# Optimization experiments

Measured on AMD Instinct MI355X. Metric: run time of the kernel, lower is better.

## Reference

```python
import jax, jax.numpy as jnp
import numpy as np

N = 4096      # num_nodes
U = 64        # num_units
IN = 2        # input_dim
DIM = U + IN  # 66
H = 4         # attention heads
ALPHA = 0.2   # leaky slope inside attention scores
SLOPE = 0.01  # nn.LeakyReLU() default for subnet activations
NEG_INF = -9e15


def setup_inputs() -> dict:
    key = jax.random.key(0)
    ks = jax.random.split(key, 20)
    def gn(k, shape, fan):
        return jax.random.normal(k, shape, dtype=jnp.float32) / np.float32(np.sqrt(fan))
    adj = jax.random.randint(ks[2], (N, N), 0, 2, dtype=jnp.int32)
    adj = jnp.maximum(adj, jnp.eye(N, dtype=jnp.int32))  # ensure self-loops
    return {
        "inputs": jax.random.normal(ks[0], (1, N * IN), dtype=jnp.float32),
        "hx": jax.random.normal(ks[1], (1, N, U), dtype=jnp.float32),
        "adj": adj,
        "m1_W": gn(ks[3], (H, DIM, DIM), DIM),
        "m1_a1": gn(ks[4], (H, DIM), DIM),
        "m1_a2": gn(ks[5], (H, DIM), DIM),
        "m1_Wout": gn(ks[6], (H * DIM, DIM), H * DIM),
        "m1_ao1": gn(ks[7], (DIM,), DIM),
        "m1_ao2": gn(ks[8], (DIM,), DIM),
        "m2_W": gn(ks[9], (H, DIM, DIM), DIM),
        "m2_a1": gn(ks[10], (H, DIM), DIM),
        "m2_a2": gn(ks[11], (H, DIM), DIM),
        "m2_Wout": gn(ks[12], (H * DIM, DIM), H * DIM),
        "m2_ao1": gn(ks[13], (DIM,), DIM),
        "m2_ao2": gn(ks[14], (DIM,), DIM),
        "g1_W": gn(ks[15], (DIM, 2 * U), DIM),
        "g1_b": jnp.zeros((2 * U,), dtype=jnp.float32),
        "g2_W": gn(ks[16], (DIM, U), DIM),
        "g2_b": jnp.zeros((U,), dtype=jnp.float32),
    }


def gat_layer(x, W, a1, a2, mask):
    # x: [N,Fin], W: [Fin,Fout], a1/a2: [Fout], mask: [N,N] bool
    h = x @ W                                   # [N,Fout]
    f1 = h @ a1                                 # [N] source term
    f2 = h @ a2                                 # [N] target term
    e = jax.nn.leaky_relu(f1[:, None] + f2[None, :], ALPHA)  # [N,N]
    e = jnp.where(mask, e, NEG_INF)
    attn = jax.nn.softmax(e, axis=-1)
    return attn @ h                             # [N,Fout]


def subnet(x, W, a1, a2, Wout, ao1, ao2, mask):
    # multi-head GAT, concat heads, activation, output GAT layer, activation
    heads = jax.vmap(gat_layer, in_axes=(None, 0, 0, 0, None))(x, W, a1, a2, mask)  # [H,N,DIM]
    hcat = jnp.transpose(heads, (1, 0, 2)).reshape(x.shape[0], -1)                   # [N,H*DIM]
    hcat = jax.nn.leaky_relu(hcat, SLOPE)
    out = gat_layer(hcat, Wout, ao1, ao2, mask)                                      # [N,DIM]
    return jax.nn.leaky_relu(out, SLOPE)


def reference(inputs, hx, adj, m1_W, m1_a1, m1_a2, m1_Wout, m1_ao1, m1_ao2,
              m2_W, m2_a1, m2_a2, m2_Wout, m2_ao1, m2_ao2,
              g1_W, g1_b, g2_W, g2_b):
    mask = adj > 0
    xi = inputs.reshape(N, IN)
    xh = hx.reshape(N, U)
    # _GAT1: concat(inputs, hx) -> GATSubNet1 -> linear -> sigmoid -> split r,u
    x1 = jnp.concatenate([xi, xh], axis=-1)                 # [N,DIM]
    g1 = subnet(x1, m1_W, m1_a1, m1_a2, m1_Wout, m1_ao1, m1_ao2, mask)
    value = jax.nn.sigmoid(g1 @ g1_W + g1_b)                # [N,2U]
    r, u = value[:, :U], value[:, U:]
    # _GAT2: concat(inputs, r*hx) -> GATSubNet2 -> linear -> tanh
    x2 = jnp.concatenate([xi, r * xh], axis=-1)             # [N,DIM]
    g2 = subnet(x2, m2_W, m2_a1, m2_a2, m2_Wout, m2_ao1, m2_ao2, mask)
    c = jnp.tanh(g2 @ g2_W + g2_b)                          # [N,U]
    new_state = u * xh + (1.0 - u) * c
    return new_state.reshape(1, N, U)
```

## Files before the change

kernel.cpp:

```cpp
#include <hip/hip_runtime.h>
#include <hip/hip_bf16.h>

constexpr int kN = 4096;
constexpr int kDim = 66;
constexpr int kH = 4;
constexpr int kU = 64;
constexpr float kAlpha = 0.2f;
constexpr float kSlope = 0.01f;
constexpr float kLog2e = 1.44269504f;

typedef _Float16 half8 __attribute__((ext_vector_type(8)));
typedef _Float16 half2t __attribute__((ext_vector_type(2)));
typedef __attribute__((ext_vector_type(4))) float floatx4;

__device__ inline unsigned int fkey(float f){
  unsigned int u = __float_as_uint(f);
  return (u & 0x80000000u) ? ~u : (u | 0x80000000u);
}
__device__ inline float funkey(unsigned int k){
  unsigned int u = (k & 0x80000000u) ? (k ^ 0x80000000u) : ~k;
  return __uint_as_float(u);
}

__global__ void setup_k(const int* __restrict__ adj, unsigned long long* __restrict__ packed,
                        const float* __restrict__ in2, const float* __restrict__ hx,
                        _Float16* __restrict__ x1b, _Float16* __restrict__ x2b,
                        const float* __restrict__ m1W, const float* __restrict__ m1a1, const float* __restrict__ m1a2,
                        const float* __restrict__ m1Wo, const float* __restrict__ m1ao1, const float* __restrict__ m1ao2,
                        const float* __restrict__ m2W, const float* __restrict__ m2a1, const float* __restrict__ m2a2,
                        const float* __restrict__ m2Wo, const float* __restrict__ m2ao1, const float* __restrict__ m2ao2,
                        const float* __restrict__ g1W, const float* __restrict__ g1b,
                        const float* __restrict__ g2W, const float* __restrict__ g2b,
                        _Float16* __restrict__ B1t, _Float16* __restrict__ B1t2,
                        _Float16* __restrict__ B2t, _Float16* __restrict__ B2t2,
                        _Float16* __restrict__ Bgt, _Float16* __restrict__ Bft,
                        unsigned int* __restrict__ fmaxbuf){
  int bb = blockIdx.x, t = threadIdx.x;
  if (bb < 16384){
    int gid = bb * 256 + t;
    unsigned long long m = __ballot(adj[gid] != 0);
    if ((t & 63) == 0) packed[gid >> 6] = m;
    return;
  }
  if (bb < 16384 + 1024){
    int i = (bb - 16384) * 4 + (t >> 6);
    int c = t & 63;
    x1b[(size_t)i * 96 + 2 + c] = (_Float16)hx[(size_t)i * kU + c];
    if (c < 2){
      _Float16 xv = (_Float16)in2[i * 2 + c];
      x1b[(size_t)i * 96 + c] = xv;
      x2b[(size_t)i * 96 + c] = xv;
    }
    if (c < 30){
      x1b[(size_t)i * 96 + 66 + c] = (_Float16)0.f;
      x2b[(size_t)i * 96 + 66 + c] = (_Float16)0.f;
    }
    return;
  }
  int b = bb - (16384 + 1024);
  if (b < 8){
    int m = b & 3;
    const float* W  = (b < 4 ? m1W  : m2W)  + (size_t)m * kDim * kDim;
    const float* a1 = (b < 4 ? m1a1 : m2a1) + m * kDim;
    const float* a2 = (b < 4 ? m1a2 : m2a2) + m * kDim;
    _Float16* Bo = (b < 4 ? B1t : B1t2) + (size_t)m * 80 * 96;
    __shared__ float Ws[kDim * kDim];
    __shared__ float wa1s[kDim], wa2s[kDim];
    for (int z = t; z < kDim * kDim; z += 256) Ws[z] = W[z];
    __syncthreads();
    if (t < kDim){
      float s1 = 0.f, s2 = 0.f;
      for (int d = 0; d < kDim; d++){ float wv = Ws[t * kDim + d]; s1 += wv * a1[d]; s2 += wv * a2[d]; }
      wa1s[t] = s1; wa2s[t] = s2;
    }
    __syncthreads();
    for (int z = t; z < 80 * 96; z += 256){
      int nn = z / 96, k = z % 96;
      float val = 0.f;
      if (k < kDim){
        if (nn < kDim) val = Ws[k * kDim + nn];
        else if (nn == 66) val = wa1s[k];
        else if (nn == 67) val = wa2s[k];
      }
      Bo[z] = (_Float16)val;
    }
  } else if (b < 10){
    const float* Wo  = (b == 8 ? m1Wo  : m2Wo);
    const float* ao1 = (b == 8 ? m1ao1 : m2ao1);
    const float* ao2 = (b == 8 ? m1ao2 : m2ao2);
    _Float16* Bo = (b == 8 ? B2t : B2t2);
    __shared__ float wo1s[264], wo2s[264];
    for (int k = t; k < 264; k += 256){
      float s1 = 0.f, s2 = 0.f;
      for (int d = 0; d < kDim; d++){ float wv = Wo[(size_t)k * kDim + d]; s1 += wv * ao1[d]; s2 += wv * ao2[d]; }
      wo1s[k] = s1; wo2s[k] = s2;
    }
    __syncthreads();
    for (int z = t; z < 80 * 288; z += 256){
      int nn = z / 288, k = z % 288;
      float val = 0.f;
      if (k < 264){
        if (nn < kDim) val = Wo[(size_t)k * kDim + nn];
        else if (nn == 66) val = wo1s[k];
        else if (nn == 67) val = wo2s[k];
      }
      Bo[z] = (_Float16)val;
    }
  } else if (b == 10){
    for (int z = t; z < 128 * 96; z += 256){
      int nn = z / 96, k = z % 96;
      float val = 0.f;
      if (k < kDim) val = g1W[k * 128 + nn];
      else if (k == 66) val = g1b[nn];
      Bgt[z] = (_Float16)val;
    }
  } else {
    if (t < 16) fmaxbuf[t] = 0u;
    for (int z = t; z < 64 * 96; z += 256){
      int nn = z / 96, k = z % 96;
      float val = 0.f;
      if (k < kDim) val = g2W[k * 64 + nn];
      else if (k == 66) val = g2b[nn];
      Bft[z] = (_Float16)val;
    }
  }
}

template<int KSTEPS, int NT, int EPI>
__global__ __launch_bounds__(256) void gemm_k(
    const _Float16* __restrict__ A, const _Float16* __restrict__ Bt,
    void* __restrict__ p0, void* __restrict__ p1, void* __restrict__ p2,
    const float* __restrict__ aux, unsigned int* __restrict__ fmaxp)
{
  constexpr int KP = KSTEPS * 32;
  const int m = blockIdx.y;
  const int i0 = blockIdx.x * 64;
  const int t = threadIdx.x;
  const int w = t >> 6, lane = t & 63, q = lane >> 4, n = lane & 15;
  const int arow = i0 + w * 16 + n;
  const _Float16* Ar = A + (size_t)arow * KP;
  const _Float16* Bm = Bt + (size_t)m * (NT * 16) * KP;
  floatx4 acc[NT];
  #pragma unroll
  for (int v = 0; v < NT; v++) acc[v] = (floatx4){0.f, 0.f, 0.f, 0.f};
  #pragma unroll
  for (int ks = 0; ks < KSTEPS; ks++){
    half8 af = *(const half8*)&Ar[ks * 32 + q * 8];
    #pragma unroll
    for (int nt = 0; nt < NT; nt++){
      half8 bf = *(const half8*)&Bm[(size_t)(nt * 16 + n) * KP + ks * 32 + q * 8];
      acc[nt] = __builtin_amdgcn_mfma_f32_16x16x32_f16(af, bf, acc[nt], 0, 0, 0);
    }
  }
  const int ib = i0 + w * 16 + q * 4;
  if constexpr (EPI == 0){
    _Float16* Ht = (_Float16*)p0 + (size_t)m * 68 * kN;
    float* f1 = (float*)p1 + (size_t)m * kN;
    float* f2 = (float*)p2 + (size_t)m * kN;
    float lm = -3e38f;
    #pragma unroll
    for (int nt = 0; nt < NT; nt++){
      int c = nt * 16 + n;
      if (c < kDim){
        union { _Float16 h[4]; uint2 v; } pk;
        pk.h[0] = (_Float16)acc[nt][0]; pk.h[1] = (_Float16)acc[nt][1];
        pk.h[2] = (_Float16)acc[nt][2]; pk.h[3] = (_Float16)acc[nt][3];
        *(uint2*)&Ht[(size_t)c * kN + ib] = pk.v;
      } else if (c == 66){
        float4 fv; fv.x = acc[nt][0] * kLog2e; fv.y = acc[nt][1] * kLog2e;
        fv.z = acc[nt][2] * kLog2e; fv.w = acc[nt][3] * kLog2e;
        *(float4*)&f1[ib] = fv;
        *(uint2*)&Ht[(size_t)66 * kN + ib] = make_uint2(0x3C003C00u, 0x3C003C00u);
      } else if (c == 67){
        float4 fv; fv.x = acc[nt][0] * kLog2e; fv.y = acc[nt][1] * kLog2e;
        fv.z = acc[nt][2] * kLog2e; fv.w = acc[nt][3] * kLog2e;
        *(float4*)&f2[ib] = fv;
        lm = fmaxf(fmaxf(fv.x, fv.y), fmaxf(fv.z, fv.w));
        *(uint2*)&Ht[(size_t)67 * kN + ib] = make_uint2(0u, 0u);
      }
    }
    lm = fmaxf(lm, __shfl_xor(lm, 16));
    lm = fmaxf(lm, __shfl_xor(lm, 32));
    if (lane == 3) atomicMax(&fmaxp[m], fkey(lm));
  } else if constexpr (EPI == 1){
    float* u = (float*)p0;
    _Float16* x2b = (_Float16*)p1;
    #pragma unroll
    for (int nt = 0; nt < NT; nt++){
      int c = nt * 16 + n;
      #pragma unroll
      for (int r = 0; r < 4; r++){
        float v = 1.f / (1.f + __expf(-acc[nt][r]));
        if (c < 64) x2b[(size_t)(ib + r) * 96 + 2 + c] = (_Float16)(v * aux[(size_t)(ib + r) * kU + c]);
        else        u[(size_t)(ib + r) * kU + (c - 64)] = v;
      }
    }
  } else {
    float* outp = (float*)p0;
    const float* u = (const float*)p1;
    #pragma unroll
    for (int nt = 0; nt < NT; nt++){
      int c = nt * 16 + n;
      #pragma unroll
      for (int r = 0; r < 4; r++){
        float cc = tanhf(acc[nt][r]);
        float uv = u[(size_t)(ib + r) * kU + c];
        outp[(size_t)(ib + r) * kU + c] = uv * aux[(size_t)(ib + r) * kU + c] + (1.f - uv) * cc;
      }
    }
  }
}

template<int JSPLIT>
__global__ __launch_bounds__(256, 4) void attn_mfma_k(
    const _Float16* __restrict__ Ht, const float* __restrict__ f1,
    const float* __restrict__ f2, const unsigned int* __restrict__ fmaxu,
    const unsigned long long* __restrict__ packed,
    _Float16* __restrict__ paccb)
{
  constexpr int JR = kN / JSPLIT;
  constexpr int NCH = JR / 128;
  const int m = blockIdx.y, js = blockIdx.z;
  const int i0 = blockIdx.x * 64;
  const int t = threadIdx.x;
  const int w = t >> 6, lane = t & 63, q = lane >> 4, n = lane & 15;
  const int i = i0 + w * 16 + n;
  const _Float16* Hg = Ht + (size_t)m * 68 * kN;
  const float* f2m = f2 + (size_t)m * kN;
  const float f1v = f1[(size_t)m * kN + i];
  const float fmx = funkey(fmaxu[m]);
  const float t0 = f1v + fmx;
  const float S = fmaxf(t0, kAlpha * t0);
  const float A1f = __builtin_amdgcn_exp2f(t0 - S);
  const float A2f = __builtin_amdgcn_exp2f(kAlpha * t0 - S);
  const half2t a1p = { (_Float16)A1f, (_Float16)A1f };
  const half2t a2p = { (_Float16)A2f, (_Float16)A2f };

  __shared__ __align__(16) _Float16 HtL[80 * 136];
  __shared__ __align__(16) _Float16 B1h[128], B2h[128];

  for (int z = t; z < 12 * 136; z += 256) HtL[68 * 136 + z] = (_Float16)0.f;

  floatx4 acc[5];
  #pragma unroll
  for (int v = 0; v < 5; v++) acc[v] = (floatx4){0.f, 0.f, 0.f, 0.f};

  const int jbase = js * JR;
  const unsigned long long* prow = packed + (size_t)i * 64;
  for (int ch = 0; ch < NCH; ch++){
    const int j0 = jbase + ch * 128;
    __syncthreads();
    for (int z = t; z < 68 * 16; z += 256){
      int row = z >> 4, c16 = z & 15;
      *(uint4*)&HtL[row * 136 + c16 * 8] = *(const uint4*)&Hg[(size_t)row * kN + j0 + c16 * 8];
    }
    if (t < 128){
      float v = f2m[j0 + t] - fmx;
      B1h[t] = (_Float16)__builtin_amdgcn_exp2f(v);
      B2h[t] = (_Float16)__builtin_amdgcn_exp2f(kAlpha * v);
    }
    __syncthreads();
    unsigned long long w0 = prow[(j0 >> 6)];
    unsigned long long w1 = prow[(j0 >> 6) + 1];
    #pragma unroll
    for (int ks = 0; ks < 4; ks++){
      unsigned long long wsel = (ks < 2) ? w0 : w1;
      unsigned int bits = (unsigned int)((wsel >> ((ks & 1) * 32 + q * 8)) & 0xffull);
      union { uint4 v; unsigned int u[4]; } b1v, b2v;
      b1v.v = *(const uint4*)&B1h[ks * 32 + q * 8];
      b2v.v = *(const uint4*)&B2h[ks * 32 + q * 8];
      union { half8 s; unsigned int u[4]; } af;
      #pragma unroll
      for (int e = 0; e < 4; e++){
        half2t x1 = __builtin_bit_cast(half2t, b1v.u[e]);
        half2t x2 = __builtin_bit_cast(half2t, b2v.u[e]);
        half2t m1 = x1 * a1p;
        half2t m2 = x2 * a2p;
        half2t pm = __builtin_elementwise_max(m1, m2);
        unsigned int mm = (((bits >> (2 * e)) & 1u) ? 0x0000FFFFu : 0u)
                        | (((bits >> (2 * e + 1)) & 1u) ? 0xFFFF0000u : 0u);
        af.u[e] = __builtin_bit_cast(unsigned int, pm) & mm;
      }
      #pragma unroll
      for (int nt = 0; nt < 5; nt++){
        const half8 bf = *(const half8*)&HtL[(nt * 16 + n) * 136 + ks * 32 + q * 8];
        acc[nt] = __builtin_amdgcn_mfma_f32_16x16x32_f16(af.s, bf, acc[nt], 0, 0, 0);
      }
    }
  }
  _Float16* pw = paccb + ((size_t)(m * JSPLIT + js) * kN + (i0 + w * 16)) * 80;
  #pragma unroll
  for (int nt = 0; nt < 5; nt++){
    if (nt < 4 || n < 4){
      #pragma unroll
      for (int r = 0; r < 4; r++)
        pw[(q * 4 + r) * 80 + nt * 16 + n] = (_Float16)acc[nt][r];
    }
  }
}

template<int JSPLIT>
__global__ void combine_k(const _Float16* __restrict__ paccb, _Float16* __restrict__ outb,
                          int ostride, int ones_col){
  int m = blockIdx.y;
  int i = blockIdx.x * 64 + (threadIdx.x >> 2);
  int cg = threadIdx.x & 3;
  const _Float16* ps[JSPLIT];
  #pragma unroll
  for (int s = 0; s < JSPLIT; s++)
    ps[s] = paccb + ((size_t)(m * JSPLIT + s) * kN + i) * 80;
  float l = 0.f;
  #pragma unroll
  for (int s = 0; s < JSPLIT; s++) l += (float)ps[s][66];
  float inv = 1.f / l;
  _Float16* orow = outb + (size_t)i * ostride + m * kDim;
  #pragma unroll
  for (int cc = 0; cc < 17; cc++){
    int c = cg * 17 + cc;
    if (c < kDim){
      float v = 0.f;
      #pragma unroll
      for (int s = 0; s < JSPLIT; s++) v += (float)ps[s][c];
      v *= inv;
      v = fmaxf(v, kSlope * v);
      orow[c] = (_Float16)v;
    }
  }
  if (ones_col && cg == 3) orow[66] = (_Float16)1.f;
}

extern "C" void kernel_launch(void* const* d_in, const int* in_sizes, int n_in,
                              void* d_out, int out_size, void* d_ws, size_t ws_size,
                              hipStream_t stream){
  const float* inputs  = (const float*)d_in[0];
  const float* hx      = (const float*)d_in[1];
  const int*   adj     = (const int*)d_in[2];
  const float* m1_W    = (const float*)d_in[3];
  const float* m1_a1   = (const float*)d_in[4];
  const float* m1_a2   = (const float*)d_in[5];
  const float* m1_Wout = (const float*)d_in[6];
  const float* m1_ao1  = (const float*)d_in[7];
  const float* m1_ao2  = (const float*)d_in[8];
  const float* m2_W    = (const float*)d_in[9];
  const float* m2_a1   = (const float*)d_in[10];
  const float* m2_a2   = (const float*)d_in[11];
  const float* m2_Wout = (const float*)d_in[12];
  const float* m2_ao1  = (const float*)d_in[13];
  const float* m2_ao2  = (const float*)d_in[14];
  const float* g1_W    = (const float*)d_in[15];
  const float* g1_b    = (const float*)d_in[16];
  const float* g2_W    = (const float*)d_in[17];
  const float* g2_b    = (const float*)d_in[18];
  float* out = (float*)d_out;

  char* ws = (char*)d_ws;
  size_t off = 0;
  auto alloc = [&](size_t bytes) -> void* {
    void* p = ws + off;
    off = (off + bytes + 255) & ~(size_t)255;
    return p;
  };
  unsigned long long* packed = (unsigned long long*)alloc((size_t)kN * 64 * 8);
  _Float16* x1b  = (_Float16*)alloc((size_t)kN * 96 * 2);
  _Float16* x2b  = (_Float16*)alloc((size_t)kN * 96 * 2);
  _Float16* Ht   = (_Float16*)alloc((size_t)kH * 68 * kN * 2);
  _Float16* Hto  = (_Float16*)alloc((size_t)68 * kN * 2);
  _Float16* hcatb= (_Float16*)alloc((size_t)kN * 288 * 2);
  _Float16* gb   = (_Float16*)alloc((size_t)kN * 96 * 2);
  _Float16* g2bv = (_Float16*)alloc((size_t)kN * 96 * 2);
  float* f1   = (float*)alloc((size_t)kH * kN * 4);
  float* f2   = (float*)alloc((size_t)kH * kN * 4);
  float* fo1  = (float*)alloc((size_t)kN * 4);
  float* fo2  = (float*)alloc((size_t)kN * 4);
  unsigned int* fmaxbuf = (unsigned int*)alloc(64);
  float* u    = (float*)alloc((size_t)kN * kU * 4);
  _Float16* paccb = (_Float16*)alloc((size_t)16 * kN * 80 * 2);
  _Float16* B1t  = (_Float16*)alloc((size_t)kH * 80 * 96 * 2);
  _Float16* B1t2 = (_Float16*)alloc((size_t)kH * 80 * 96 * 2);
  _Float16* B2t  = (_Float16*)alloc((size_t)80 * 288 * 2);
  _Float16* B2t2 = (_Float16*)alloc((size_t)80 * 288 * 2);
  _Float16* Bgt  = (_Float16*)alloc((size_t)128 * 96 * 2);
  _Float16* Bft  = (_Float16*)alloc((size_t)64 * 96 * 2);
  (void)ws_size; (void)in_sizes; (void)n_in; (void)out_size;

  setup_k<<<16384 + 1024 + 12, 256, 0, stream>>>(adj, packed, inputs, hx, x1b, x2b,
      m1_W, m1_a1, m1_a2, m1_Wout, m1_ao1, m1_ao2,
      m2_W, m2_a1, m2_a2, m2_Wout, m2_ao1, m2_ao2,
      g1_W, g1_b, g2_W, g2_b,
      B1t, B1t2, B2t, B2t2, Bgt, Bft, fmaxbuf);

  gemm_k<3, 5, 0><<<dim3(64, kH), 256, 0, stream>>>(x1b, B1t, Ht, f1, f2, nullptr, fmaxbuf + 0);
  attn_mfma_k<4><<<dim3(64, kH, 4), 256, 0, stream>>>(Ht, f1, f2, fmaxbuf + 0, packed, paccb);
  combine_k<4><<<dim3(64, kH), 256, 0, stream>>>(paccb, hcatb, 288, 0);
  gemm_k<9, 5, 0><<<dim3(64, 1), 256, 0, stream>>>(hcatb, B2t, Hto, fo1, fo2, nullptr, fmaxbuf + 4);
  attn_mfma_k<8><<<dim3(64, 1, 8), 256, 0, stream>>>(Hto, fo1, fo2, fmaxbuf + 4, packed, paccb);
  combine_k<8><<<dim3(64, 1), 256, 0, stream>>>(paccb, gb, 96, 1);
  gemm_k<3, 8, 1><<<dim3(64, 1), 256, 0, stream>>>(gb, Bgt, u, x2b, nullptr, hx, nullptr);

  gemm_k<3, 5, 0><<<dim3(64, kH), 256, 0, stream>>>(x2b, B1t2, Ht, f1, f2, nullptr, fmaxbuf + 5);
  attn_mfma_k<4><<<dim3(64, kH, 4), 256, 0, stream>>>(Ht, f1, f2, fmaxbuf + 5, packed, paccb);
  combine_k<4><<<dim3(64, kH), 256, 0, stream>>>(paccb, hcatb, 288, 0);
  gemm_k<9, 5, 0><<<dim3(64, 1), 256, 0, stream>>>(hcatb, B2t2, Hto, fo1, fo2, nullptr, fmaxbuf + 9);
  attn_mfma_k<8><<<dim3(64, 1, 8), 256, 0, stream>>>(Hto, fo1, fo2, fmaxbuf + 9, packed, paccb);
  combine_k<8><<<dim3(64, 1), 256, 0, stream>>>(paccb, g2bv, 96, 1);
  gemm_k<3, 4, 2><<<dim3(64, 1), 256, 0, stream>>>(g2bv, Bft, out, u, nullptr, hx, nullptr);
}
```

Before: 321.3 us.

## Fuse split-K combine into following GEMMs via LDS and widen output-layer split

Merges each combine kernel into the next GEMM: the partial attention sums are reduced, normalized and activated straight into LDS, then fed to the MFMA GEMM, so the hcat/gb intermediates never go to global memory and four launches are removed. The partial-accumulator row stride shrinks from 80 to 72 halves, and the output-layer attention split goes from 8 to 16 so more blocks run. The fused kernels launch only 64 blocks, and the wider split means more partial traffic to reduce.

```diff
diff --git a/kernel.cpp b/kernel.cpp
--- a/kernel.cpp
+++ b/kernel.cpp
@@ -1,9 +1,7 @@
 #include <hip/hip_runtime.h>
-#include <hip/hip_bf16.h>
 
 constexpr int kN = 4096;
 constexpr int kDim = 66;
-constexpr int kH = 4;
 constexpr int kU = 64;
 constexpr float kAlpha = 0.2f;
 constexpr float kSlope = 0.01f;
@@ -11,7 +9,7 @@
 
 typedef _Float16 half8 __attribute__((ext_vector_type(8)));
 typedef _Float16 half2t __attribute__((ext_vector_type(2)));
-typedef __attribute__((ext_vector_type(4))) float floatx4;
+typedef float floatx4 __attribute__((ext_vector_type(4)));
 
 __device__ inline unsigned int fkey(float f){
   unsigned int u = __float_as_uint(f);
@@ -126,89 +124,66 @@
   }
 }
 
-template<int KSTEPS, int NT, int EPI>
-__global__ __launch_bounds__(256) void gemm_k(
-    const _Float16* __restrict__ A, const _Float16* __restrict__ Bt,
-    void* __restrict__ p0, void* __restrict__ p1, void* __restrict__ p2,
-    const float* __restrict__ aux, unsigned int* __restrict__ fmaxp)
-{
-  constexpr int KP = KSTEPS * 32;
-  const int m = blockIdx.y;
-  const int i0 = blockIdx.x * 64;
-  const int t = threadIdx.x;
-  const int w = t >> 6, lane = t & 63, q = lane >> 4, n = lane & 15;
-  const int arow = i0 + w * 16 + n;
-  const _Float16* Ar = A + (size_t)arow * KP;
-  const _Float16* Bm = Bt + (size_t)m * (NT * 16) * KP;
-  floatx4 acc[NT];
+template<int KSTEPS, int NT>
+__device__ __forceinline__ void gemmN(const _Float16* __restrict__ Arow,
+                                      const _Float16* __restrict__ Bt, floatx4* acc){
+  const int lane = threadIdx.x & 63, q = lane >> 4, n = lane & 15;
   #pragma unroll
   for (int v = 0; v < NT; v++) acc[v] = (floatx4){0.f, 0.f, 0.f, 0.f};
   #pragma unroll
   for (int ks = 0; ks < KSTEPS; ks++){
-    half8 af = *(const half8*)&Ar[ks * 32 + q * 8];
+    half8 af = *(const half8*)&Arow[ks * 32 + q * 8];
     #pragma unroll
     for (int nt = 0; nt < NT; nt++){
-      half8 bf = *(const half8*)&Bm[(size_t)(nt * 16 + n) * KP + ks * 32 + q * 8];
+      half8 bf = *(const half8*)&Bt[(size_t)(nt * 16 + n) * (KSTEPS * 32) + ks * 32 + q * 8];
       acc[nt] = __builtin_amdgcn_mfma_f32_16x16x32_f16(af, bf, acc[nt], 0, 0, 0);
     }
   }
+}
+
+__device__ __forceinline__ void epi0(floatx4* acc, int i0, _Float16* __restrict__ Htc,
+                                     float* __restrict__ f1c, float* __restrict__ f2c,
+                                     unsigned* __restrict__ fmaxslot){
+  const int t = threadIdx.x, w = t >> 6, lane = t & 63, q = lane >> 4, n = lane & 15;
   const int ib = i0 + w * 16 + q * 4;
-  if constexpr (EPI == 0){
-    _Float16* Ht = (_Float16*)p0 + (size_t)m * 68 * kN;
-    float* f1 = (float*)p1 + (size_t)m * kN;
-    float* f2 = (float*)p2 + (size_t)m * kN;
-    float lm = -3e38f;
-    #pragma unroll
-    for (int nt = 0; nt < NT; nt++){
-      int c = nt * 16 + n;
-      if (c < kDim){
-        union { _Float16 h[4]; uint2 v; } pk;
-        pk.h[0] = (_Float16)acc[nt][0]; pk.h[1] = (_Float16)acc[nt][1];
-        pk.h[2] = (_Float16)acc[nt][2]; pk.h[3] = (_Float16)acc[nt][3];
-        *(uint2*)&Ht[(size_t)c * kN + ib] = pk.v;
-      } else if (c == 66){
-        float4 fv; fv.x = acc[nt][0] * kLog2e; fv.y = acc[nt][1] * kLog2e;
-        fv.z = acc[nt][2] * kLog2e; fv.w = acc[nt][3] * kLog2e;
-        *(float4*)&f1[ib] = fv;
-        *(uint2*)&Ht[(size_t)66 * kN + ib] = make_uint2(0x3C003C00u, 0x3C003C00u);
-      } else if (c == 67){
-        float4 fv; fv.x = acc[nt][0] * kLog2e; fv.y = acc[nt][1] * kLog2e;
-        fv.z = acc[nt][2] * kLog2e; fv.w = acc[nt][3] * kLog2e;
-        *(float4*)&f2[ib] = fv;
-        lm = fmaxf(fmaxf(fv.x, fv.y), fmaxf(fv.z, fv.w));
-        *(uint2*)&Ht[(size_t)67 * kN + ib] = make_uint2(0u, 0u);
-      }
-    }
-    lm = fmaxf(lm, __shfl_xor(lm, 16));
-    lm = fmaxf(lm, __shfl_xor(lm, 32));
-    if (lane == 3) atomicMax(&fmaxp[m], fkey(lm));
-  } else if constexpr (EPI == 1){
-    float* u = (float*)p0;
-    _Float16* x2b = (_Float16*)p1;
-    #pragma unroll
-    for (int nt = 0; nt < NT; nt++){
-      int c = nt * 16 + n;
-      #pragma unroll
-      for (int r = 0; r < 4; r++){
-        float v = 1.f / (1.f + __expf(-acc[nt][r]));
-        if (c < 64) x2b[(size_t)(ib + r) * 96 + 2 + c] = (_Float16)(v * aux[(size_t)(ib + r) * kU + c]);
-        else        u[(size_t)(ib + r) * kU + (c - 64)] = v;
-      }
-    }
-  } else {
-    float* outp = (float*)p0;
-    const float* u = (const float*)p1;
-    #pragma unroll
-    for (int nt = 0; nt < NT; nt++){
-      int c = nt * 16 + n;
-      #pragma unroll
-      for (int r = 0; r < 4; r++){
-        float cc = tanhf(acc[nt][r]);
-        float uv = u[(size_t)(ib + r) * kU + c];
-        outp[(size_t)(ib + r) * kU + c] = uv * aux[(size_t)(ib + r) * kU + c] + (1.f - uv) * cc;
-      }
-    }
-  }
+  float lm = -3e38f;
+  #pragma unroll
+  for (int nt = 0; nt < 5; nt++){
+    int c = nt * 16 + n;
+    if (c < kDim){
+      union { _Float16 h[4]; uint2 v; } pk;
+      pk.h[0] = (_Float16)acc[nt][0]; pk.h[1] = (_Float16)acc[nt][1];
+      pk.h[2] = (_Float16)acc[nt][2]; pk.h[3] = (_Float16)acc[nt][3];
+      *(uint2*)&Htc[(size_t)c * kN + ib] = pk.v;
+    } else if (c == 66){
+      float4 fv; fv.x = acc[nt][0] * kLog2e; fv.y = acc[nt][1] * kLog2e;
+      fv.z = acc[nt][2] * kLog2e; fv.w = acc[nt][3] * kLog2e;
+      *(float4*)&f1c[ib] = fv;
+      *(uint2*)&Htc[(size_t)66 * kN + ib] = make_uint2(0x3C003C00u, 0x3C003C00u);
+    } else if (c == 67){
+      float4 fv; fv.x = acc[nt][0] * kLog2e; fv.y = acc[nt][1] * kLog2e;
+      fv.z = acc[nt][2] * kLog2e; fv.w = acc[nt][3] * kLog2e;
+      *(float4*)&f2c[ib] = fv;
+      lm = fmaxf(fmaxf(fv.x, fv.y), fmaxf(fv.z, fv.w));
+      *(uint2*)&Htc[(size_t)67 * kN + ib] = make_uint2(0u, 0u);
+    }
+  }
+  lm = fmaxf(lm, __shfl_xor(lm, 16));
+  lm = fmaxf(lm, __shfl_xor(lm, 32));
+  if (lane == 3) atomicMax(fmaxslot, fkey(lm));
+}
+
+__global__ __launch_bounds__(256) void gemm_ht_k(
+    const _Float16* __restrict__ A, const _Float16* __restrict__ Bt,
+    _Float16* __restrict__ Ht, float* __restrict__ f1, float* __restrict__ f2,
+    unsigned int* __restrict__ fmaxp)
+{
+  const int m = blockIdx.y;
+  const int i0 = blockIdx.x * 64;
+  const int w = threadIdx.x >> 6, n = threadIdx.x & 15;
+  floatx4 acc[5];
+  gemmN<3, 5>(A + (size_t)(i0 + w * 16 + n) * 96, Bt + (size_t)m * 80 * 96, acc);
+  epi0(acc, i0, Ht + (size_t)m * 68 * kN, f1 + (size_t)m * kN, f2 + (size_t)m * kN, fmaxp + m);
 }
 
 template<int JSPLIT>
@@ -288,45 +263,125 @@
       }
     }
   }
-  _Float16* pw = paccb + ((size_t)(m * JSPLIT + js) * kN + (i0 + w * 16)) * 80;
+  _Float16* pw = paccb + ((size_t)(m * JSPLIT + js) * kN + (i0 + w * 16)) * 72;
   #pragma unroll
   for (int nt = 0; nt < 5; nt++){
     if (nt < 4 || n < 4){
       #pragma unroll
       for (int r = 0; r < 4; r++)
-        pw[(q * 4 + r) * 80 + nt * 16 + n] = (_Float16)acc[nt][r];
-    }
-  }
-}
-
-template<int JSPLIT>
-__global__ void combine_k(const _Float16* __restrict__ paccb, _Float16* __restrict__ outb,
-                          int ostride, int ones_col){
-  int m = blockIdx.y;
-  int i = blockIdx.x * 64 + (threadIdx.x >> 2);
-  int cg = threadIdx.x & 3;
-  const _Float16* ps[JSPLIT];
-  #pragma unroll
-  for (int s = 0; s < JSPLIT; s++)
-    ps[s] = paccb + ((size_t)(m * JSPLIT + s) * kN + i) * 80;
-  float l = 0.f;
-  #pragma unroll
-  for (int s = 0; s < JSPLIT; s++) l += (float)ps[s][66];
-  float inv = 1.f / l;
-  _Float16* orow = outb + (size_t)i * ostride + m * kDim;
-  #pragma unroll
-  for (int cc = 0; cc < 17; cc++){
-    int c = cg * 17 + cc;
-    if (c < kDim){
-      float v = 0.f;
-      #pragma unroll
-      for (int s = 0; s < JSPLIT; s++) v += (float)ps[s][c];
-      v *= inv;
-      v = fmaxf(v, kSlope * v);
-      orow[c] = (_Float16)v;
-    }
-  }
-  if (ones_col && cg == 3) orow[66] = (_Float16)1.f;
+        pw[(q * 4 + r) * 72 + nt * 16 + n] = (_Float16)acc[nt][r];
+    }
+  }
+}
+
+__global__ __launch_bounds__(256) void combineH_gemmO_k(
+    const _Float16* __restrict__ pacc, const _Float16* __restrict__ B2tc,
+    _Float16* __restrict__ Htoc, float* __restrict__ fo1c, float* __restrict__ fo2c,
+    unsigned int* __restrict__ fmaxslot)
+{
+  __shared__ __align__(16) _Float16 hcatL[64 * 296];
+  const int t = threadIdx.x;
+  const int i0 = blockIdx.x * 64;
+  {
+    const int mm = t >> 6, row = t & 63;
+    const _Float16* pb = pacc + ((size_t)(mm * 4) * kN + (i0 + row)) * 72;
+    constexpr size_t jstep = (size_t)kN * 72;
+    float l = 0.f;
+    #pragma unroll
+    for (int s = 0; s < 4; s++) l += (float)pb[s * jstep + 66];
+    float inv = 1.f / l;
+    _Float16* hr = hcatL + row * 296 + mm * 66;
+    #pragma unroll
+    for (int c8 = 0; c8 < 9; c8++){
+      float sv[8] = {0.f,0.f,0.f,0.f,0.f,0.f,0.f,0.f};
+      #pragma unroll
+      for (int s = 0; s < 4; s++){
+        half8 hv = *(const half8*)&pb[s * jstep + c8 * 8];
+        #pragma unroll
+        for (int e = 0; e < 8; e++) sv[e] += (float)hv[e];
+      }
+      #pragma unroll
+      for (int e = 0; e < 8; e++){
+        int c = c8 * 8 + e;
+        if (c < kDim){
+          float vv = sv[e] * inv;
+          vv = fmaxf(vv, kSlope * vv);
+          hr[c] = (_Float16)vv;
+        }
+      }
+    }
+  }
+  for (int z = t; z < 64 * 32; z += 256)
+    hcatL[(z >> 5) * 296 + 264 + (z & 31)] = (_Float16)0.f;
+  __syncthreads();
+  const int w = t >> 6, n = t & 15;
+  floatx4 acc[5];
+  gemmN<9, 5>(hcatL + (w * 16 + n) * 296, B2tc, acc);
+  epi0(acc, i0, Htoc, fo1c, fo2c, fmaxslot);
+}
+
+template<int EPI>
+__global__ __launch_bounds__(256) void combineO_gemm_k(
+    const _Float16* __restrict__ pacc, const _Float16* __restrict__ Btc,
+    float* __restrict__ uv, const float* __restrict__ hxp,
+    _Float16* __restrict__ x2bp, float* __restrict__ outp)
+{
+  __shared__ __align__(16) _Float16 gbL[64 * 104];
+  const int t = threadIdx.x;
+  const int i0 = blockIdx.x * 64;
+  {
+    const int row = t >> 2, cg = t & 3;
+    const _Float16* pb = pacc + (size_t)(i0 + row) * 72;
+    constexpr size_t jstep = (size_t)kN * 72;
+    float l = 0.f;
+    #pragma unroll
+    for (int s = 0; s < 16; s++) l += (float)pb[s * jstep + 66];
+    float inv = 1.f / l;
+    _Float16* gr = gbL + row * 104;
+    for (int cc = 0; cc < 17; cc++){
+      int c = cg * 17 + cc;
+      if (c < kDim){
+        float vv = 0.f;
+        #pragma unroll
+        for (int s = 0; s < 16; s++) vv += (float)pb[s * jstep + c];
+        vv *= inv; vv = fmaxf(vv, kSlope * vv);
+        gr[c] = (_Float16)vv;
+      } else if (c == 66) gr[66] = (_Float16)1.f;
+      else if (c == 67) gr[67] = (_Float16)0.f;
+    }
+    #pragma unroll
+    for (int e = 0; e < 9; e++) gr[68 + cg * 9 + e] = (_Float16)0.f;
+  }
+  __syncthreads();
+  const int w = t >> 6, lane = t & 63, q = lane >> 4, n = lane & 15;
+  const int ib = i0 + w * 16 + q * 4;
+  if constexpr (EPI == 1){
+    floatx4 acc[8];
+    gemmN<3, 8>(gbL + (w * 16 + n) * 104, Btc, acc);
+    #pragma unroll
+    for (int nt = 0; nt < 8; nt++){
+      int c = nt * 16 + n;
+      #pragma unroll
+      for (int r = 0; r < 4; r++){
+        float v = 1.f / (1.f + __expf(-acc[nt][r]));
+        if (c < 64) x2bp[(size_t)(ib + r) * 96 + 2 + c] = (_Float16)(v * hxp[(size_t)(ib + r) * kU + c]);
+        else        uv[(size_t)(ib + r) * kU + (c - 64)] = v;
+      }
+    }
+  } else {
+    floatx4 acc[4];
+    gemmN<3, 4>(gbL + (w * 16 + n) * 104, Btc, acc);
+    #pragma unroll
+    for (int nt = 0; nt < 4; nt++){
+      int c = nt * 16 + n;
+      #pragma unroll
+      for (int r = 0; r < 4; r++){
+        float cc2 = tanhf(acc[nt][r]);
+        float u2 = uv[(size_t)(ib + r) * kU + c];
+        outp[(size_t)(ib + r) * kU + c] = u2 * hxp[(size_t)(ib + r) * kU + c] + (1.f - u2) * cc2;
+      }
+    }
+  }
 }
 
 extern "C" void kernel_launch(void* const* d_in, const int* in_sizes, int n_in,
@@ -363,20 +418,17 @@
   unsigned long long* packed = (unsigned long long*)alloc((size_t)kN * 64 * 8);
   _Float16* x1b  = (_Float16*)alloc((size_t)kN * 96 * 2);
   _Float16* x2b  = (_Float16*)alloc((size_t)kN * 96 * 2);
-  _Float16* Ht   = (_Float16*)alloc((size_t)kH * 68 * kN * 2);
+  _Float16* Ht   = (_Float16*)alloc((size_t)4 * 68 * kN * 2);
   _Float16* Hto  = (_Float16*)alloc((size_t)68 * kN * 2);
-  _Float16* hcatb= (_Float16*)alloc((size_t)kN * 288 * 2);
-  _Float16* gb   = (_Float16*)alloc((size_t)kN * 96 * 2);
-  _Float16* g2bv = (_Float16*)alloc((size_t)kN * 96 * 2);
-  float* f1   = (float*)alloc((size_t)kH * kN * 4);
-  float* f2   = (float*)alloc((size_t)kH * kN * 4);
+  float* f1   = (float*)alloc((size_t)4 * kN * 4);
+  float* f2   = (float*)alloc((size_t)4 * kN * 4);
   float* fo1  = (float*)alloc((size_t)kN * 4);
   float* fo2  = (float*)alloc((size_t)kN * 4);
   unsigned int* fmaxbuf = (unsigned int*)alloc(64);
   float* u    = (float*)alloc((size_t)kN * kU * 4);
-  _Float16* paccb = (_Float16*)alloc((size_t)16 * kN * 80 * 2);
-  _Float16* B1t  = (_Float16*)alloc((size_t)kH * 80 * 96 * 2);
-  _Float16* B1t2 = (_Float16*)alloc((size_t)kH * 80 * 96 * 2);
+  _Float16* pacc = (_Float16*)alloc((size_t)16 * kN * 72 * 2);
+  _Float16* B1t  = (_Float16*)alloc((size_t)4 * 80 * 96 * 2);
+  _Float16* B1t2 = (_Float16*)alloc((size_t)4 * 80 * 96 * 2);
   _Float16* B2t  = (_Float16*)alloc((size_t)80 * 288 * 2);
   _Float16* B2t2 = (_Float16*)alloc((size_t)80 * 288 * 2);
   _Float16* Bgt  = (_Float16*)alloc((size_t)128 * 96 * 2);
@@ -389,19 +441,15 @@
       g1_W, g1_b, g2_W, g2_b,
       B1t, B1t2, B2t, B2t2, Bgt, Bft, fmaxbuf);
 
-  gemm_k<3, 5, 0><<<dim3(64, kH), 256, 0, stream>>>(x1b, B1t, Ht, f1, f2, nullptr, fmaxbuf + 0);
-  attn_mfma_k<4><<<dim3(64, kH, 4), 256, 0, stream>>>(Ht, f1, f2, fmaxbuf + 0, packed, paccb);
-  combine_k<4><<<dim3(64, kH), 256, 0, stream>>>(paccb, hcatb, 288, 0);
-  gemm_k<9, 5, 0><<<dim3(64, 1), 256, 0, stream>>>(hcatb, B2t, Hto, fo1, fo2, nullptr, fmaxbuf + 4);
-  attn_mfma_k<8><<<dim3(64, 1, 8), 256, 0, stream>>>(Hto, fo1, fo2, fmaxbuf + 4, packed, paccb);
-  combine_k<8><<<dim3(64, 1), 256, 0, stream>>>(paccb, gb, 96, 1);
-  gemm_k<3, 8, 1><<<dim3(64, 1), 256, 0, stream>>>(gb, Bgt, u, x2b, nullptr, hx, nullptr);
-
-  gemm_k<3, 5, 0><<<dim3(64, kH), 256, 0, stream>>>(x2b, B1t2, Ht, f1, f2, nullptr, fmaxbuf + 5);
-  attn_mfma_k<4><<<dim3(64, kH, 4), 256, 0, stream>>>(Ht, f1, f2, fmaxbuf + 5, packed, paccb);
-  combine_k<4><<<dim3(64, kH), 256, 0, stream>>>(paccb, hcatb, 288, 0);
-  gemm_k<9, 5, 0><<<dim3(64, 1), 256, 0, stream>>>(hcatb, B2t2, Hto, fo1, fo2, nullptr, fmaxbuf + 9);
-  attn_mfma_k<8><<<dim3(64, 1, 8), 256, 0, stream>>>(Hto, fo1, fo2, fmaxbuf + 9, packed, paccb);
-  combine_k<8><<<dim3(64, 1), 256, 0, stream>>>(paccb, g2bv, 96, 1);
-  gemm_k<3, 4, 2><<<dim3(64, 1), 256, 0, stream>>>(g2bv, Bft, out, u, nullptr, hx, nullptr);
-}
+  gemm_ht_k<<<dim3(64, 4), 256, 0, stream>>>(x1b, B1t, Ht, f1, f2, fmaxbuf + 0);
+  attn_mfma_k<4><<<dim3(64, 4, 4), 256, 0, stream>>>(Ht, f1, f2, fmaxbuf + 0, packed, pacc);
+  combineH_gemmO_k<<<64, 256, 0, stream>>>(pacc, B2t, Hto, fo1, fo2, fmaxbuf + 4);
+  attn_mfma_k<16><<<dim3(64, 1, 16), 256, 0, stream>>>(Hto, fo1, fo2, fmaxbuf + 4, packed, pacc);
+  combineO_gemm_k<1><<<64, 256, 0, stream>>>(pacc, Bgt, u, hx, x2b, nullptr);
+
+  gemm_ht_k<<<dim3(64, 4), 256, 0, stream>>>(x2b, B1t2, Ht, f1, f2, fmaxbuf + 5);
+  attn_mfma_k<4><<<dim3(64, 4, 4), 256, 0, stream>>>(Ht, f1, f2, fmaxbuf + 5, packed, pacc);
+  combineH_gemmO_k<<<64, 256, 0, stream>>>(pacc, B2t2, Hto, fo1, fo2, fmaxbuf + 9);
+  attn_mfma_k<16><<<dim3(64, 1, 16), 256, 0, stream>>>(Hto, fo1, fo2, fmaxbuf + 9, packed, pacc);
+  combineO_gemm_k<2><<<64, 256, 0, stream>>>(pacc, Bft, u, hx, nullptr, out);
+}
```

New measurement: 322.8 us. No clear change (+0.5%).
